# Kernel tuning notes

Measured on AMD Instinct MI355X. Metric: run time of the kernel, lower is better.

## Reference

```python
import jax, jax.numpy as jnp
import numpy as np

D_MODEL = 1024
D_INNER = 2048      # expand=2 * d_model
HEADDIM = 64
NHEADS = D_INNER // HEADDIM   # 32 (ssm heads)
D_STATE = 128
D_CONV = 4
CHUNK = 256
D_IN_PROJ = 2 * D_INNER + 2 * D_STATE + NHEADS
CONV_DIM = D_INNER + 2 * D_STATE


def setup_inputs() -> dict:
    key = jax.random.key(0)
    ks = jax.random.split(key, 8)
    sc = lambda f: 1.0 / np.sqrt(f)
    dt_init = jax.random.uniform(ks[3], (NHEADS,), minval=0.001, maxval=0.1)
    return {
        "x": jax.random.normal(ks[0], (2, 4096, D_MODEL), jnp.float32),
        "W_in": jax.random.normal(ks[1], (D_MODEL, D_IN_PROJ), jnp.float32) * sc(D_MODEL),
        "conv_w": jax.random.normal(ks[2], (CONV_DIM, D_CONV), jnp.float32) * sc(D_CONV),
        "conv_b": jnp.zeros((CONV_DIM,), jnp.float32),
        "dt_bias": jnp.log(jnp.expm1(dt_init)),            # inverse softplus
        "A_log": jnp.log(jax.random.uniform(ks[4], (NHEADS,), minval=1.0, maxval=16.0)),
        "D": jnp.ones((NHEADS,), jnp.float32),
        "norm_w": jnp.ones((D_INNER,), jnp.float32),
        "W_out": jax.random.normal(ks[5], (D_INNER, D_MODEL), jnp.float32) * sc(D_INNER),
    }


def _segsum(a):
    # a: (..., T) -> (..., T, T) lower-triangular segment sums, -inf above diag
    T = a.shape[-1]
    cs = jnp.cumsum(a, axis=-1)
    diff = cs[..., :, None] - cs[..., None, :]
    mask = jnp.tril(jnp.ones((T, T), bool))
    return jnp.where(mask, diff, -jnp.inf)


def _ssd(x, A, B, C):
    # x: (b,L,h,p) already scaled by dt; A: (b,L,h) = dt*A_head; B,C: (b,L,n)
    b, L, h, p = x.shape
    nc = L // CHUNK
    xc = x.reshape(b, nc, CHUNK, h, p)
    Ac = A.reshape(b, nc, CHUNK, h).transpose(0, 3, 1, 2)      # (b,h,nc,cl)
    Bc = B.reshape(b, nc, CHUNK, -1)
    Cc = C.reshape(b, nc, CHUNK, -1)
    Acs = jnp.cumsum(Ac, axis=-1)
    # intra-chunk (diagonal) term
    Ldec = jnp.exp(_segsum(Ac))                                # (b,h,nc,cl,cl)
    Yd = jnp.einsum('bcln,bcsn,bhcls,bcshp->bclhp', Cc, Bc, Ldec, xc)
    # chunk end states
    decay_states = jnp.exp(Acs[..., -1:] - Acs)                # (b,h,nc,cl)
    states = jnp.einsum('bcln,bhcl,bclhp->bchpn', Bc, decay_states, xc)
    # inter-chunk recurrence (zero initial state)
    states = jnp.concatenate([jnp.zeros_like(states[:, :1]), states], axis=1)
    A_chunk = jnp.pad(Acs[..., -1], ((0, 0), (0, 0), (1, 0)))  # (b,h,nc+1)
    decay_chunk = jnp.exp(_segsum(A_chunk))                    # (b,h,nc+1,nc+1)
    states = jnp.einsum('bhzc,bchpn->bzhpn', decay_chunk, states)[:, :-1]
    # state -> output term
    out_decay = jnp.exp(Acs)                                   # (b,h,nc,cl)
    Yo = jnp.einsum('bcln,bchpn,bhcl->bclhp', Cc, states, out_decay)
    return (Yd + Yo).reshape(b, L, h, p)


def reference(x, W_in, conv_w, conv_b, dt_bias, A_log, D, norm_w, W_out):
    b, L, _ = x.shape
    zxbcdt = x @ W_in                                          # (b,L,4384)
    z, xBC, dt = jnp.split(zxbcdt, [D_INNER, 2 * D_INNER + 2 * D_STATE], axis=-1)
    # causal depthwise conv1d + silu
    xp = jnp.pad(xBC, ((0, 0), (D_CONV - 1, 0), (0, 0)))
    conv = sum(xp[:, k:k + L] * conv_w[:, k] for k in range(D_CONV)) + conv_b
    xBC = jax.nn.silu(conv)
    xs, B, C = jnp.split(xBC, [D_INNER, D_INNER + D_STATE], axis=-1)
    dt = jax.nn.softplus(dt + dt_bias)                         # (b,L,h)
    A = -jnp.exp(A_log)                                        # (h,)
    xh = xs.reshape(b, L, NHEADS, HEADDIM)
    y = _ssd(xh * dt[..., None], dt * A, B, C)                 # (b,L,h,p)
    y = y + xh * D[None, None, :, None]                        # D skip per head
    y = y.reshape(b, L, D_INNER)
    # gated RMSNorm
    u = y * jax.nn.silu(z)
    u = u * jax.lax.rsqrt(jnp.mean(u * u, axis=-1, keepdims=True) + 1e-5) * norm_w
    return u @ W_out
```

## Files before the change

### kernel.cpp

```cpp
#include <hip/hip_runtime.h>
#include <math.h>

#define B_ 2
#define L_ 4096
#define DM 1024
#define DI 2048
#define HD 64
#define NH 32
#define DS 128
#define CH 256
#define NC 16
#define DPROJ 4384
#define CONVD 2304
#define NGEMM 4352

typedef unsigned short u16;
typedef unsigned int u32;
typedef __attribute__((ext_vector_type(8))) short bf16x8;
typedef __attribute__((ext_vector_type(4))) float f32x4;

__device__ __forceinline__ float silu_(float x) { return x / (1.0f + __expf(-x)); }
__device__ __forceinline__ float us2f(u16 u) {
  union { u32 i; float f; } c; c.i = ((u32)u) << 16; return c.f;
}
__device__ __forceinline__ u16 f2us(float f) {
  union { float f; u32 i; } c; c.f = f;
  u32 i = c.i;
  return (u16)((i + 0x7FFFu + ((i >> 16) & 1u)) >> 16);
}
__device__ __forceinline__ void unpack8(uint4 v, float* o) {
  o[0] = us2f(v.x & 0xffffu); o[1] = us2f(v.x >> 16);
  o[2] = us2f(v.y & 0xffffu); o[3] = us2f(v.y >> 16);
  o[4] = us2f(v.z & 0xffffu); o[5] = us2f(v.z >> 16);
  o[6] = us2f(v.w & 0xffffu); o[7] = us2f(v.w >> 16);
}
__device__ __forceinline__ void unpk16(uint4 v, u16* o) {
  o[0] = (u16)(v.x & 0xffffu); o[1] = (u16)(v.x >> 16);
  o[2] = (u16)(v.y & 0xffffu); o[3] = (u16)(v.y >> 16);
  o[4] = (u16)(v.z & 0xffffu); o[5] = (u16)(v.z >> 16);
  o[6] = (u16)(v.w & 0xffffu); o[7] = (u16)(v.w >> 16);
}
__device__ __forceinline__ bf16x8 scale8(bf16x8 a, float s) {
  bf16x8 r;
#pragma unroll
  for (int j = 0; j < 8; ++j) r[j] = (short)f2us(us2f((u16)a[j]) * s);
  return r;
}
__device__ __forceinline__ void gload16(const u16* g, u16* l) {
  __builtin_amdgcn_global_load_lds(
      (const __attribute__((address_space(1))) void*)g,
      (__attribute__((address_space(3))) void*)l, 16, 0, 0);
}

__global__ __launch_bounds__(256) void cvt_t_k(const float* __restrict__ W,
                                               u16* __restrict__ Wt,
                                               int ldW, int ldT) {
  __shared__ float tile[64][65];
  const int t = threadIdx.x;
  const int n0 = blockIdx.x * 64, k0 = blockIdx.y * 64;
#pragma unroll
  for (int i = 0; i < 16; ++i) {
    int j = i * 256 + t;
    int kk = j >> 6, nn = j & 63;
    tile[kk][nn] = W[(size_t)(k0 + kk) * ldW + n0 + nn];
  }
  __syncthreads();
#pragma unroll
  for (int i = 0; i < 16; ++i) {
    int j = i * 256 + t;
    int nn = j >> 6, kk = j & 63;
    Wt[(size_t)(n0 + nn) * ldT + k0 + kk] = f2us(tile[kk][nn]);
  }
}

__global__ __launch_bounds__(256) void cvt_tw_k(const float* __restrict__ W,
                                                const float* __restrict__ nw,
                                                u16* __restrict__ Wt,
                                                int ldW, int ldT) {
  __shared__ float tile[64][65];
  const int t = threadIdx.x;
  const int n0 = blockIdx.x * 64, k0 = blockIdx.y * 64;
#pragma unroll
  for (int i = 0; i < 16; ++i) {
    int j = i * 256 + t;
    int kk = j >> 6, nn = j & 63;
    tile[kk][nn] = W[(size_t)(k0 + kk) * ldW + n0 + nn] * nw[k0 + kk];
  }
  __syncthreads();
#pragma unroll
  for (int i = 0; i < 16; ++i) {
    int j = i * 256 + t;
    int nn = j >> 6, kk = j & 63;
    Wt[(size_t)(n0 + nn) * ldT + k0 + kk] = f2us(tile[kk][nn]);
  }
}

__global__ __launch_bounds__(512, 4) void gemm_in_k(const u16* __restrict__ A,
                                                    const u16* __restrict__ Bt,
                                                    u16* __restrict__ zb,
                                                    u16* __restrict__ xraw,
                                                    int nwg) {
  __shared__ u16 pool[24576];
  u16* Al = pool;
  u16* Bl = pool + 16384;
  const int t = threadIdx.x;
  const int w = t >> 6, lane = t & 63;
  const int fr = lane & 15, oct = lane >> 4;
  const int wm = w >> 1, wn = w & 1;
  const int q = nwg >> 3;
  const int wg = (blockIdx.x & 7) * q + (blockIdx.x >> 3);
  const int bm = wg / (NGEMM / 128), bn = wg % (NGEMM / 128);
  const int m0 = bm * 256, n0 = bn * 128;
  const int lr = lane >> 3, ls = lane & 7;
  const int gslot = (ls ^ lr) * 8;

  f32x4 acc[4][4];
#pragma unroll
  for (int mm = 0; mm < 4; ++mm)
#pragma unroll
    for (int nn = 0; nn < 4; ++nn) acc[mm][nn] = (f32x4){0.f, 0.f, 0.f, 0.f};

  for (int k0 = 0; k0 < DM; k0 += 64) {
    if (k0) __syncthreads();
#pragma unroll
    for (int i = 0; i < 4; ++i) {
      const int rowA = w * 32 + i * 8;
      gload16(&A[(size_t)(m0 + rowA + lr) * DM + k0 + gslot], &Al[rowA * 64]);
    }
#pragma unroll
    for (int i = 0; i < 2; ++i) {
      const int rowB = w * 16 + i * 8;
      gload16(&Bt[(size_t)(n0 + rowB + lr) * DM + k0 + gslot], &Bl[rowB * 64]);
    }
    __syncthreads();
#pragma unroll
    for (int kk = 0; kk < 2; ++kk) {
      bf16x8 af[4], bfr[4];
#pragma unroll
      for (int mm = 0; mm < 4; ++mm)
        af[mm] = *(const bf16x8*)&Al[(wm * 64 + mm * 16 + fr) * 64 +
                                     (((kk * 4 + oct) ^ (fr & 7)) * 8)];
#pragma unroll
      for (int nn = 0; nn < 4; ++nn)
        bfr[nn] = *(const bf16x8*)&Bl[(wn * 64 + nn * 16 + fr) * 64 +
                                      (((kk * 4 + oct) ^ (fr & 7)) * 8)];
      __builtin_amdgcn_s_setprio(1);
#pragma unroll
      for (int mm = 0; mm < 4; ++mm)
#pragma unroll
        for (int nn = 0; nn < 4; ++nn)
          acc[mm][nn] = __builtin_amdgcn_mfma_f32_16x16x32_bf16(af[mm], bfr[nn],
                                                                acc[mm][nn], 0, 0, 0);
      __builtin_amdgcn_s_setprio(0);
    }
  }

  const bool isz = (n0 < DI);
  u16* Oh = pool;
#pragma unroll
  for (int P = 0; P < 4; ++P) {
    __syncthreads();
    if (wm == P) {
#pragma unroll
      for (int mm = 0; mm < 4; ++mm)
#pragma unroll
        for (int i = 0; i < 4; ++i) {
          int rloc = mm * 16 + oct * 4 + i;
#pragma unroll
          for (int nn = 0; nn < 4; ++nn)
            Oh[rloc * 136 + wn * 64 + nn * 16 + fr] = f2us(acc[mm][nn][i]);
        }
    }
    __syncthreads();
#pragma unroll
    for (int p = 0; p < 2; ++p) {
      int e = p * 512 + t;
      int row = e >> 4, cs = (e & 15) * 8;
      uint4 v = *(const uint4*)&Oh[row * 136 + cs];
      size_t grow = m0 + P * 64 + row;
      int col = n0 + cs;
      if (isz) *(uint4*)&zb[grow * DI + col] = v;
      else     *(uint4*)&xraw[grow * CONVD + (col - DI)] = v;
    }
  }
}

template <int KDIM, int NTN>
__global__ __launch_bounds__(256) void gemm_bf16_k(const u16* __restrict__ A,
                                                   const u16* __restrict__ Bt,
                                                   const float* __restrict__ rowsum,
                                                   float* __restrict__ outf,
                                                   int nwg) {
  __shared__ u16 pool[17408];
  u16* Al = pool;
  u16* Bl = pool + 8192;
  const int t = threadIdx.x;
  const int wv = t >> 6, lane = t & 63;
  const int fr = lane & 15, oct = lane >> 4;
  const int wr = wv >> 1, wc = wv & 1;
  const int q = nwg >> 3;
  const int wg = (blockIdx.x & 7) * q + (blockIdx.x >> 3);
  const int bm = wg / NTN, bn = wg % NTN;
  const int m0 = bm * 128, n0 = bn * 128;

  const int lr = lane >> 3, ls = lane & 7;
  const int gslot = (ls ^ lr) * 8;

  f32x4 acc[4][4];
#pragma unroll
  for (int mm = 0; mm < 4; ++mm)
#pragma unroll
    for (int nn = 0; nn < 4; ++nn) acc[mm][nn] = (f32x4){0.f, 0.f, 0.f, 0.f};

  for (int k0 = 0; k0 < KDIM; k0 += 64) {
    if (k0) __syncthreads();
#pragma unroll
    for (int i = 0; i < 4; ++i) {
      const int rowA = wv * 32 + i * 8;
      gload16(&A[(size_t)(m0 + rowA + lr) * KDIM + k0 + gslot], &Al[rowA * 64]);
      gload16(&Bt[(size_t)(n0 + rowA + lr) * KDIM + k0 + gslot], &Bl[rowA * 64]);
    }
    __syncthreads();
#pragma unroll
    for (int kk = 0; kk < 2; ++kk) {
      bf16x8 af[4], bfr[4];
#pragma unroll
      for (int mm = 0; mm < 4; ++mm)
        af[mm] = *(const bf16x8*)&Al[(wr * 64 + mm * 16 + fr) * 64 +
                                     (((kk * 4 + oct) ^ (fr & 7)) * 8)];
#pragma unroll
      for (int nn = 0; nn < 4; ++nn)
        bfr[nn] = *(const bf16x8*)&Bl[(wc * 64 + nn * 16 + fr) * 64 +
                                      (((kk * 4 + oct) ^ (fr & 7)) * 8)];
#pragma unroll
      for (int mm = 0; mm < 4; ++mm)
#pragma unroll
        for (int nn = 0; nn < 4; ++nn)
          acc[mm][nn] = __builtin_amdgcn_mfma_f32_16x16x32_bf16(af[mm], bfr[nn],
                                                                acc[mm][nn], 0, 0, 0);
    }
  }

#pragma unroll
  for (int P = 0; P < 2; ++P) {
    __syncthreads();
    float* Of = (float*)pool;
    if (wr == P) {
#pragma unroll
      for (int mm = 0; mm < 4; ++mm)
#pragma unroll
        for (int i = 0; i < 4; ++i) {
          int rloc = mm * 16 + oct * 4 + i;
#pragma unroll
          for (int nn = 0; nn < 4; ++nn)
            Of[rloc * 132 + wc * 64 + nn * 16 + fr] = acc[mm][nn][i];
        }
    }
    __syncthreads();
#pragma unroll
    for (int p = 0; p < 8; ++p) {
      int e = p * 256 + t;
      int row = e >> 5, c4 = (e & 31) * 4;
      size_t grow = m0 + P * 64 + row;
      float s = rsqrtf(rowsum[grow] * (1.0f / DI) + 1e-5f);
      float4 v = *(const float4*)&Of[row * 132 + c4];
      v.x *= s; v.y *= s; v.z *= s; v.w *= s;
      *(float4*)&outf[grow * DM + n0 + c4] = v;
    }
  }
}

__global__ __launch_bounds__(256) void rowsum_k(const float* __restrict__ psum,
                                                float* __restrict__ rowsum) {
  int row = blockIdx.x * 256 + threadIdx.x;
  const float4* p = (const float4*)&psum[(size_t)row * 32];
  float s = 0.0f;
#pragma unroll
  for (int i = 0; i < 8; ++i) {
    float4 v = p[i];
    s += (v.x + v.y) + (v.z + v.w);
  }
  rowsum[row] = s;
}

__global__ __launch_bounds__(256) void dt_gemm_k(const float* __restrict__ x,
                                                 const float* __restrict__ W,
                                                 const float* __restrict__ dtb,
                                                 float* __restrict__ dtp,
                                                 u16* __restrict__ xb16) {
  __shared__ float xs[8 * 1024];
  const int t = threadIdx.x;
  const int row0 = blockIdx.x * 8;
#pragma unroll
  for (int i = 0; i < 8; ++i) {
    int j4 = i * 256 + t;
    float4 v = *(const float4*)&x[(size_t)row0 * DM + j4 * 4];
    *(float4*)&xs[j4 * 4] = v;
    u32 lo = (u32)f2us(v.x) | ((u32)f2us(v.y) << 16);
    u32 hi = (u32)f2us(v.z) | ((u32)f2us(v.w) << 16);
    *(uint2*)&xb16[(size_t)row0 * DM + j4 * 4] = make_uint2(lo, hi);
  }
  __syncthreads();
  const int r = t >> 5, h = t & 31;
  float a0 = 0.f, a1 = 0.f, a2 = 0.f, a3 = 0.f;
  const float* wcol = W + (DI + CONVD) + h;
  const float* xr = &xs[r * 1024];
  for (int k = 0; k < 1024; k += 4) {
    float4 xv = *(const float4*)&xr[k];
    a0 += xv.x * wcol[(size_t)(k + 0) * DPROJ];
    a1 += xv.y * wcol[(size_t)(k + 1) * DPROJ];
    a2 += xv.z * wcol[(size_t)(k + 2) * DPROJ];
    a3 += xv.w * wcol[(size_t)(k + 3) * DPROJ];
  }
  float v = (a0 + a1) + (a2 + a3) + dtb[h];
  dtp[(size_t)(row0 + r) * NH + h] = (v > 20.0f) ? v : log1pf(__expf(v));
}

__global__ __launch_bounds__(256) void conv_silu_k(const u16* __restrict__ xraw,
                                                   const float* __restrict__ cw,
                                                   const float* __restrict__ cb,
                                                   u16* __restrict__ xbc) {
  int idx = blockIdx.x * 256 + threadIdx.x;
  int ch8 = idx % (CONVD / 8);
  int bl = idx / (CONVD / 8);
  int l = bl & (L_ - 1);
  int ch = ch8 * 8;
  const u16* src = xraw + (size_t)bl * CONVD + ch;
  float a[8], o[8];
#pragma unroll
  for (int qq = 0; qq < 8; ++qq) a[qq] = cb[ch + qq];
  float w0[8], w1[8], w2[8], w3[8];
#pragma unroll
  for (int qq = 0; qq < 8; ++qq) {
    float4 w = *(const float4*)&cw[(ch + qq) * 4];
    w0[qq] = w.x; w1[qq] = w.y; w2[qq] = w.z; w3[qq] = w.w;
  }
  if (l >= 3) {
    uint4 v = *(const uint4*)&src[-3 * CONVD]; unpack8(v, o);
#pragma unroll
    for (int qq = 0; qq < 8; ++qq) a[qq] += o[qq] * w0[qq];
  }
  if (l >= 2) {
    uint4 v = *(const uint4*)&src[-2 * CONVD]; unpack8(v, o);
#pragma unroll
    for (int qq = 0; qq < 8; ++qq) a[qq] += o[qq] * w1[qq];
  }
  if (l >= 1) {
    uint4 v = *(const uint4*)&src[-CONVD]; unpack8(v, o);
#pragma unroll
    for (int qq = 0; qq < 8; ++qq) a[qq] += o[qq] * w2[qq];
  }
  {
    uint4 v = *(const uint4*)&src[0]; unpack8(v, o);
#pragma unroll
    for (int qq = 0; qq < 8; ++qq) a[qq] += o[qq] * w3[qq];
  }
  uint4 ov;
  ov.x = (u32)f2us(silu_(a[0])) | ((u32)f2us(silu_(a[1])) << 16);
  ov.y = (u32)f2us(silu_(a[2])) | ((u32)f2us(silu_(a[3])) << 16);
  ov.z = (u32)f2us(silu_(a[4])) | ((u32)f2us(silu_(a[5])) << 16);
  ov.w = (u32)f2us(silu_(a[6])) | ((u32)f2us(silu_(a[7])) << 16);
  *(uint4*)&xbc[(size_t)bl * CONVD + ch] = ov;
}

__global__ __launch_bounds__(256) void acs_k(const float* __restrict__ dtp,
                                             const float* __restrict__ A_log,
                                             float* __restrict__ Acs) {
  const int t = threadIdx.x;
  const int lane = t & 63, wv = t >> 6;
  const int idx = blockIdx.x * 4 + wv;
  const int h = (idx >> 4) & (NH - 1);
  const int c = idx & (NC - 1);
  const int b = idx >> 9;
  const float Ah = -__expf(A_log[h]);
  const size_t base = ((size_t)b * L_ + c * CH + lane * 4) * NH + h;
  float v0 = dtp[base] * Ah;
  float v1 = dtp[base + NH] * Ah;
  float v2 = dtp[base + 2 * NH] * Ah;
  float v3 = dtp[base + 3 * NH] * Ah;
  float c1 = v0 + v1, c2 = c1 + v2, c3 = c2 + v3;
  float tot = c3;
#pragma unroll
  for (int off = 1; off < 64; off <<= 1) {
    float p = __shfl_up(tot, off, 64);
    if (lane >= off) tot += p;
  }
  float excl = tot - c3;
  float4 ov = make_float4(excl + v0, excl + c1, excl + c2, excl + c3);
  *(float4*)&Acs[(size_t)idx * CH + lane * 4] = ov;
}

#define SLP 72
__global__ __launch_bounds__(256) void states_k(const u16* __restrict__ xbc,
                                                const float* __restrict__ dtp,
                                                const float* __restrict__ Acs,
                                                u16* __restrict__ st16) {
  __shared__ u16 BtT[128 * SLP];
  __shared__ u16 XtT[64 * SLP];
  const int t = threadIdx.x;
  const int wv = t >> 6, lane = t & 63;
  const int fr = lane & 15, oct = lane >> 4;
  const int sw = (blockIdx.x & 7) * 128 + (blockIdx.x >> 3);
  const int h = sw & 31, c = (sw >> 5) & 15, b = sw >> 9;
  const size_t acsb = (((size_t)b * NH + h) * NC + c) * CH;
  const float acs_last = Acs[acsb + (CH - 1)];
  const size_t rowbase = (size_t)b * L_ + c * CH;

  f32x4 acc[2][4];
#pragma unroll
  for (int mt = 0; mt < 2; ++mt)
#pragma unroll
    for (int pt = 0; pt < 4; ++pt) acc[mt][pt] = (f32x4){0.f, 0.f, 0.f, 0.f};

  for (int lt = 0; lt < 4; ++lt) {
    __syncthreads();
#pragma unroll
    for (int i = 0; i < 2; ++i) {
      int ci = i * 256 + t;
      int lp = ci >> 4, nk = ci & 15;
      int l0 = lp * 2;
      const u16* srcp = &xbc[(rowbase + lt * 64 + l0) * CONVD + DI + nk * 8];
      uint4 v0 = *(const uint4*)srcp;
      uint4 v1 = *(const uint4*)(srcp + CONVD);
      u16 a0[8], a1[8];
      unpk16(v0, a0); unpk16(v1, a1);
#pragma unroll
      for (int qq = 0; qq < 8; ++qq) {
        int r = nk * 8 + qq;
        u32 val = (u32)a0[qq] | ((u32)a1[qq] << 16);
        *(u32*)&BtT[r * SLP + ((((l0 >> 3) ^ (r >> 3)) & 7) << 3) + (l0 & 7)] = val;
      }
    }
    {
      int lp = t >> 3, pk = t & 7;
      int l0 = lp * 2;
      size_t row0 = rowbase + lt * 64 + l0;
      uint4 v0 = *(const uint4*)&xbc[row0 * CONVD + h * HD + pk * 8];
      uint4 v1 = *(const uint4*)&xbc[(row0 + 1) * CONVD + h * HD + pk * 8];
      float d0 = dtp[row0 * NH + h] * __expf(acs_last - Acs[acsb + lt * 64 + l0]);
      float d1 = dtp[(row0 + 1) * NH + h] * __expf(acs_last - Acs[acsb + lt * 64 + l0 + 1]);
      float o0[8], o1[8];
      unpack8(v0, o0); unpack8(v1, o1);
#pragma unroll
      for (int qq = 0; qq < 8; ++qq) {
        int r = pk * 8 + qq;
        u32 val = (u32)f2us(o0[qq] * d0) | ((u32)f2us(o1[qq] * d1) << 16);
        *(u32*)&XtT[r * SLP + ((((l0 >> 3) ^ (r >> 3)) & 7) << 3) + (l0 & 7)] = val;
      }
    }
    __syncthreads();
    __builtin_amdgcn_s_setprio(1);
#pragma unroll
    for (int ks = 0; ks < 2; ++ks) {
      bf16x8 afr[2], bfr[4];
#pragma unroll
      for (int mt = 0; mt < 2; ++mt) {
        int r = wv * 32 + mt * 16 + fr;
        afr[mt] = *(const bf16x8*)&BtT[r * SLP + ((((ks * 4 + oct) ^ (r >> 3)) & 7) << 3)];
      }
#pragma unroll
      for (int pt = 0; pt < 4; ++pt) {
        int r = pt * 16 + fr;
        bfr[pt] = *(const bf16x8*)&XtT[r * SLP + ((((ks * 4 + oct) ^ (r >> 3)) & 7) << 3)];
      }
#pragma unroll
      for (int mt = 0; mt < 2; ++mt)
#pragma unroll
        for (int pt = 0; pt < 4; ++pt)
          acc[mt][pt] = __builtin_amdgcn_mfma_f32_16x16x32_bf16(afr[mt], bfr[pt],
                                                                acc[mt][pt], 0, 0, 0);
    }
    __builtin_amdgcn_s_setprio(0);
  }
  size_t sbase = (((size_t)b * NC + c) * NH + h) * (size_t)(HD * DS);
#pragma unroll
  for (int mt = 0; mt < 2; ++mt)
#pragma unroll
    for (int pt = 0; pt < 4; ++pt) {
      int p = pt * 16 + fr;
      int n0 = wv * 32 + mt * 16 + oct * 4;
      u32 lo = (u32)f2us(acc[mt][pt][0]) | ((u32)f2us(acc[mt][pt][1]) << 16);
      u32 hi = (u32)f2us(acc[mt][pt][2]) | ((u32)f2us(acc[mt][pt][3]) << 16);
      *(uint2*)&st16[sbase + (size_t)p * DS + n0] = make_uint2(lo, hi);
    }
}

__global__ __launch_bounds__(256) void scan_k(u16* __restrict__ st16,
                                              const float* __restrict__ Acs) {
  const int t = threadIdx.x;
  const int seg = blockIdx.x & 15;
  const int bh = blockIdx.x >> 4;
  const int h = bh & 31, b = bh >> 5;
  const int e2 = seg * 256 + t;
  const size_t acssb = ((size_t)b * NH + h) * NC * CH;
  float run0 = 0.0f, run1 = 0.0f;
#pragma unroll
  for (int c = 0; c < NC; ++c) {
    float dAl = __expf(Acs[acssb + (size_t)c * CH + (CH - 1)]);
    size_t e = (((size_t)b * NC + c) * NH + h) * (size_t)(HD * DS) + e2 * 2;
    u32 v = *(const u32*)&st16[e];
    float s0 = us2f((u16)(v & 0xffffu)), s1 = us2f((u16)(v >> 16));
    *(u32*)&st16[e] = (u32)f2us(run0) | ((u32)f2us(run1) << 16);
    run0 = fmaf(dAl, run0, s0);
    run1 = fmaf(dAl, run1, s1);
  }
}

#define SP 72
#define XOFF 8192
#define POFF 12800
__global__ __launch_bounds__(512, 4) void ssd_out_k(const u16* __restrict__ xbc,
                                                    const float* __restrict__ dtp,
                                                    const float* __restrict__ Acs,
                                                    const u16* __restrict__ st16,
                                                    const float* __restrict__ Dvec,
                                                    const u16* __restrict__ zb,
                                                    u16* __restrict__ v_out,
                                                    float* __restrict__ psum) {
  __shared__ u16 pool[31232];
  __shared__ float acs_s[256];
  const int t = threadIdx.x;
  const int w = t >> 6, lane = t & 63;
  const int fr = lane & 15, oct = lane >> 4;
  const int sw = (blockIdx.x & 7) * 128 + (blockIdx.x >> 3);
  const int h = sw & 31, c = (sw >> 5) & 15, b = sw >> 9;
  const size_t acsb = (((size_t)b * NH + h) * NC + c) * CH;
  const size_t rowbase = (size_t)b * L_ + c * CH;
  if (t < 256) acs_s[t] = Acs[acsb + t];
  const size_t sb = (((size_t)b * NC + c) * NH + h) * (size_t)(HD * DS);
#pragma unroll
  for (int i = 0; i < 2; ++i) {
    int ci = i * 512 + t; int p = ci >> 4, nk = ci & 15;
    uint4 v = *(const uint4*)&st16[sb + (size_t)p * DS + nk * 8];
    *(uint4*)&pool[p * 136 + nk * 8] = v;
  }
  __syncthreads();
  bf16x8 ca[2][4];
#pragma unroll
  for (int mt = 0; mt < 2; ++mt)
#pragma unroll
    for (int kk = 0; kk < 4; ++kk)
      ca[mt][kk] = *(const bf16x8*)&xbc[(rowbase + w * 32 + mt * 16 + fr) * CONVD +
                                        DI + DS + kk * 32 + oct * 8];
  f32x4 acc_y[2][4];
#pragma unroll
  for (int mt = 0; mt < 2; ++mt)
#pragma unroll
    for (int pp4 = 0; pp4 < 4; ++pp4) acc_y[mt][pp4] = (f32x4){0.f, 0.f, 0.f, 0.f};

  {
    float eL0 = __expf(acs_s[w * 32 + fr]);
    float eL1 = __expf(acs_s[w * 32 + 16 + fr]);
    __builtin_amdgcn_s_setprio(1);
#pragma unroll
    for (int kk = 0; kk < 4; ++kk) {
      bf16x8 c0 = scale8(ca[0][kk], eL0);
      bf16x8 c1 = scale8(ca[1][kk], eL1);
#pragma unroll
      for (int pp4 = 0; pp4 < 4; ++pp4) {
        bf16x8 sf = *(const bf16x8*)&pool[(pp4 * 16 + fr) * 136 + kk * 32 + oct * 8];
        acc_y[0][pp4] = __builtin_amdgcn_mfma_f32_16x16x32_bf16(c0, sf, acc_y[0][pp4], 0, 0, 0);
        acc_y[1][pp4] = __builtin_amdgcn_mfma_f32_16x16x32_bf16(c1, sf, acc_y[1][pp4], 0, 0, 0);
      }
    }
    __builtin_amdgcn_s_setprio(0);
  }

  const int stmax = w >> 1, delta = (w & 1) << 5;
  for (int st = 0; st < 4; ++st) {
    __syncthreads();
#pragma unroll
    for (int i = 0; i < 2; ++i) {
      int ci = i * 512 + t; int ll = ci >> 4, ck = ci & 15;
      uint4 v = *(const uint4*)&xbc[(rowbase + st * 64 + ll) * CONVD + DI + ck * 8];
      *(uint4*)&pool[ll * 128 + ((ck * 8) ^ ((ll & 7) << 3))] = v;
    }
    if (t < 256) {
      int lp = t >> 3, pk = t & 7;
      int s0 = lp * 2;
      size_t row0 = rowbase + st * 64 + s0;
      uint4 v0 = *(const uint4*)&xbc[row0 * CONVD + h * HD + pk * 8];
      uint4 v1 = *(const uint4*)&xbc[(row0 + 1) * CONVD + h * HD + pk * 8];
      float d0 = dtp[row0 * NH + h];
      float d1 = dtp[(row0 + 1) * NH + h];
      float o0[8], o1[8];
      unpack8(v0, o0); unpack8(v1, o1);
#pragma unroll
      for (int qq = 0; qq < 8; ++qq) {
        int r = pk * 8 + qq;
        u32 val = (u32)f2us(o0[qq] * d0) | ((u32)f2us(o1[qq] * d1) << 16);
        *(u32*)&pool[XOFF + r * SP + ((((s0 >> 3) ^ (r >> 3)) & 7) << 3) + (s0 & 7)] = val;
      }
    }
    __syncthreads();
    if (st > stmax) continue;
    const bool diag = (st == stmax);
#pragma unroll
    for (int ss4 = 0; ss4 < 4; ++ss4) {
      bf16x8 bbf[4];
#pragma unroll
      for (int kk = 0; kk < 4; ++kk)
        bbf[kk] = *(const bf16x8*)&pool[(ss4 * 16 + fr) * 128 +
                                        ((kk * 32 + oct * 8) ^ ((fr & 7) << 3))];
      int s_in = ss4 * 16 + fr;
      float aS = acs_s[st * 64 + s_in];
#pragma unroll
      for (int mt = 0; mt < 2; ++mt) {
        f32x4 sacc = (f32x4){0.f, 0.f, 0.f, 0.f};
        __builtin_amdgcn_s_setprio(1);
#pragma unroll
        for (int kk = 0; kk < 4; ++kk)
          sacc = __builtin_amdgcn_mfma_f32_16x16x32_bf16(ca[mt][kk], bbf[kk], sacc, 0, 0, 0);
        __builtin_amdgcn_s_setprio(0);
#pragma unroll
        for (int i = 0; i < 4; ++i) {
          int r = mt * 16 + oct * 4 + i;
          float aL = acs_s[w * 32 + r];
          float wgt = (!diag || (s_in <= r + delta)) ? __expf(aL - aS) : 0.0f;
          pool[POFF + w * 2304 + r * SP + s_in] = f2us(sacc[i] * wgt);
        }
      }
    }
    bf16x8 pa[2][2];
#pragma unroll
    for (int mt = 0; mt < 2; ++mt)
#pragma unroll
      for (int k2 = 0; k2 < 2; ++k2)
        pa[mt][k2] = *(const bf16x8*)&pool[POFF + w * 2304 + (mt * 16 + fr) * SP +
                                           k2 * 32 + oct * 8];
    __builtin_amdgcn_s_setprio(1);
#pragma unroll
    for (int pp4 = 0; pp4 < 4; ++pp4) {
      int rx = pp4 * 16 + fr, xg = rx >> 3;
      bf16x8 xb0 = *(const bf16x8*)&pool[XOFF + rx * SP + (((oct) ^ xg) & 7) * 8];
      bf16x8 xb1 = *(const bf16x8*)&pool[XOFF + rx * SP + (((4 + oct) ^ xg) & 7) * 8];
#pragma unroll
      for (int mt = 0; mt < 2; ++mt) {
        acc_y[mt][pp4] = __builtin_amdgcn_mfma_f32_16x16x32_bf16(pa[mt][0], xb0, acc_y[mt][pp4], 0, 0, 0);
        acc_y[mt][pp4] = __builtin_amdgcn_mfma_f32_16x16x32_bf16(pa[mt][1], xb1, acc_y[mt][pp4], 0, 0, 0);
      }
    }
    __builtin_amdgcn_s_setprio(0);
  }

  const float Dh = Dvec[h];
  float rs[2][4];
#pragma unroll
  for (int mt = 0; mt < 2; ++mt)
#pragma unroll
    for (int i = 0; i < 4; ++i) {
      size_t row = rowbase + w * 32 + mt * 16 + oct * 4 + i;
      float rsum = 0.0f;
#pragma unroll
      for (int pp4 = 0; pp4 < 4; ++pp4) {
        int col = h * HD + pp4 * 16 + fr;
        float xs = us2f(xbc[row * CONVD + col]);
        float zz = us2f(zb[row * DI + col]);
        float vv = (acc_y[mt][pp4][i] + Dh * xs) * silu_(zz);
        v_out[row * DI + col] = f2us(vv);
        rsum += vv * vv;
      }
      rs[mt][i] = rsum;
    }
#pragma unroll
  for (int mt = 0; mt < 2; ++mt)
#pragma unroll
    for (int i = 0; i < 4; ++i) {
      float s = rs[mt][i];
#pragma unroll
      for (int off = 8; off >= 1; off >>= 1) s += __shfl_xor(s, off, 64);
      if (fr == 0) {
        size_t row = rowbase + w * 32 + mt * 16 + oct * 4 + i;
        psum[row * 32 + h] = s;
      }
    }
}

extern "C" void kernel_launch(void* const* d_in, const int* in_sizes, int n_in,
                              void* d_out, int out_size, void* d_ws, size_t ws_size,
                              hipStream_t stream) {
  const float* x      = (const float*)d_in[0];
  const float* W_in   = (const float*)d_in[1];
  const float* conv_w = (const float*)d_in[2];
  const float* conv_b = (const float*)d_in[3];
  const float* dt_b   = (const float*)d_in[4];
  const float* A_log  = (const float*)d_in[5];
  const float* Dvec   = (const float*)d_in[6];
  const float* norm_w = (const float*)d_in[7];
  const float* W_out  = (const float*)d_in[8];
  float* out = (float*)d_out;

  u16* zb       = (u16*)d_ws;
  u16* xbc      = zb + (size_t)B_ * L_ * DI;
  float* dtp    = (float*)(xbc + (size_t)B_ * L_ * CONVD);
  float* Acs    = dtp + (size_t)B_ * L_ * NH;
  u16* stregion = (u16*)(Acs + (size_t)B_ * NH * L_);
  u16* uni      = stregion + (size_t)B_ * NC * NH * HD * DS * 2;
  u16* xraw = uni;
  u16* v    = uni;

  u16* xb16     = stregion;
  u16* wint     = stregion + (size_t)B_ * L_ * DM;
  u16* states16 = stregion;
  float* psum   = (float*)(stregion + (size_t)B_ * NC * NH * HD * DS);
  float* rowsum = psum + (size_t)B_ * L_ * NH;
  u16* woutt    = stregion;

  const int Mrows = B_ * L_;

  dt_gemm_k<<<Mrows / 8, 256, 0, stream>>>(x, W_in, dt_b, dtp, xb16);
  cvt_t_k<<<dim3(NGEMM / 64, DM / 64), 256, 0, stream>>>(W_in, wint, DPROJ, DM);

  const int nwg_in = (Mrows / 256) * (NGEMM / 128);
  gemm_in_k<<<nwg_in, 512, 0, stream>>>(xb16, wint, zb, xraw, nwg_in);

  conv_silu_k<<<(Mrows * (CONVD / 8)) / 256, 256, 0, stream>>>(xraw, conv_w, conv_b, xbc);
  acs_k<<<(B_ * NH * NC) / 4, 256, 0, stream>>>(dtp, A_log, Acs);
  states_k<<<B_ * NC * NH, 256, 0, stream>>>(xbc, dtp, Acs, states16);
  scan_k<<<B_ * NH * 16, 256, 0, stream>>>(states16, Acs);
  ssd_out_k<<<B_ * NC * NH, 512, 0, stream>>>(xbc, dtp, Acs, states16, Dvec,
                                              zb, v, psum);
  rowsum_k<<<Mrows / 256, 256, 0, stream>>>(psum, rowsum);

  cvt_tw_k<<<dim3(DM / 64, DI / 64), 256, 0, stream>>>(W_out, norm_w, woutt, DM, DI);
  const int nwg_out = (Mrows / 128) * (DM / 128);
  gemm_bf16_k<DI, DM / 128><<<nwg_out, 256, 0, stream>>>(v, woutt, rowsum, out, nwg_out);
}
```

Measured before the change: 339.6 us.

## Merge prep kernels, fold acs into states and rowsum into output GEMM

Merges the dt GEMM, bf16 conversion of x, and both weight transposes into a single prep kernel dispatched by block index. The per-chunk cumsum (acs) moves into states_k, which keeps it in shared memory and also writes it out for later kernels. The row-sum reduction moves into the output GEMM prologue. This cuts kernel launches from 11 to 7 and removes some global round-trips. In exchange, the workspace layout changes so the transposed W_out and psum get their own regions, and states_k does redundant per-block scan work.

```diff
diff --git a/kernel.cpp b/kernel.cpp
--- a/kernel.cpp
+++ b/kernel.cpp
@@ -52,46 +52,70 @@
       (__attribute__((address_space(3))) void*)l, 16, 0, 0);
 }
 
-__global__ __launch_bounds__(256) void cvt_t_k(const float* __restrict__ W,
-                                               u16* __restrict__ Wt,
-                                               int ldW, int ldT) {
-  __shared__ float tile[64][65];
+__global__ __launch_bounds__(256) void prep_k(const float* __restrict__ x,
+                                              const float* __restrict__ W_in,
+                                              const float* __restrict__ W_out,
+                                              const float* __restrict__ nw,
+                                              const float* __restrict__ dtb,
+                                              float* __restrict__ dtp,
+                                              u16* __restrict__ xb16,
+                                              u16* __restrict__ wint,
+                                              u16* __restrict__ woutt) {
+  __shared__ float shmem[8 * 1024];
   const int t = threadIdx.x;
-  const int n0 = blockIdx.x * 64, k0 = blockIdx.y * 64;
-#pragma unroll
-  for (int i = 0; i < 16; ++i) {
-    int j = i * 256 + t;
-    int kk = j >> 6, nn = j & 63;
-    tile[kk][nn] = W[(size_t)(k0 + kk) * ldW + n0 + nn];
-  }
-  __syncthreads();
-#pragma unroll
-  for (int i = 0; i < 16; ++i) {
-    int j = i * 256 + t;
-    int nn = j >> 6, kk = j & 63;
-    Wt[(size_t)(n0 + nn) * ldT + k0 + kk] = f2us(tile[kk][nn]);
-  }
-}
-
-__global__ __launch_bounds__(256) void cvt_tw_k(const float* __restrict__ W,
-                                                const float* __restrict__ nw,
-                                                u16* __restrict__ Wt,
-                                                int ldW, int ldT) {
-  __shared__ float tile[64][65];
-  const int t = threadIdx.x;
-  const int n0 = blockIdx.x * 64, k0 = blockIdx.y * 64;
-#pragma unroll
-  for (int i = 0; i < 16; ++i) {
-    int j = i * 256 + t;
-    int kk = j >> 6, nn = j & 63;
-    tile[kk][nn] = W[(size_t)(k0 + kk) * ldW + n0 + nn] * nw[k0 + kk];
-  }
-  __syncthreads();
-#pragma unroll
-  for (int i = 0; i < 16; ++i) {
-    int j = i * 256 + t;
-    int nn = j >> 6, kk = j & 63;
-    Wt[(size_t)(n0 + nn) * ldT + k0 + kk] = f2us(tile[kk][nn]);
+  const int bid = blockIdx.x;
+  if (bid < 1024) {
+    const int row0 = bid * 8;
+#pragma unroll
+    for (int i = 0; i < 8; ++i) {
+      int j4 = i * 256 + t;
+      float4 v = *(const float4*)&x[(size_t)row0 * DM + j4 * 4];
+      *(float4*)&shmem[j4 * 4] = v;
+      u32 lo = (u32)f2us(v.x) | ((u32)f2us(v.y) << 16);
+      u32 hi = (u32)f2us(v.z) | ((u32)f2us(v.w) << 16);
+      *(uint2*)&xb16[(size_t)row0 * DM + j4 * 4] = make_uint2(lo, hi);
+    }
+    __syncthreads();
+    const int r = t >> 5, h = t & 31;
+    float a0 = 0.f, a1 = 0.f, a2 = 0.f, a3 = 0.f;
+    const float* wcol = W_in + (DI + CONVD) + h;
+    const float* xr = &shmem[r * 1024];
+    for (int k = 0; k < 1024; k += 4) {
+      float4 xv = *(const float4*)&xr[k];
+      a0 += xv.x * wcol[(size_t)(k + 0) * DPROJ];
+      a1 += xv.y * wcol[(size_t)(k + 1) * DPROJ];
+      a2 += xv.z * wcol[(size_t)(k + 2) * DPROJ];
+      a3 += xv.w * wcol[(size_t)(k + 3) * DPROJ];
+    }
+    float v = (a0 + a1) + (a2 + a3) + dtb[h];
+    dtp[(size_t)(row0 + r) * NH + h] = (v > 20.0f) ? v : log1pf(__expf(v));
+  } else {
+    float (*tile)[65] = (float(*)[65])shmem;
+    const float* W; u16* Wt; int ldW, ldT, n0, k0; bool fold;
+    if (bid < 2112) {
+      int j = bid - 1024;
+      W = W_in; Wt = wint; ldW = DPROJ; ldT = DM; fold = false;
+      n0 = (j % (NGEMM / 64)) * 64; k0 = (j / (NGEMM / 64)) * 64;
+    } else {
+      int j = bid - 2112;
+      W = W_out; Wt = woutt; ldW = DM; ldT = DI; fold = true;
+      n0 = (j % (DM / 64)) * 64; k0 = (j / (DM / 64)) * 64;
+    }
+#pragma unroll
+    for (int i = 0; i < 16; ++i) {
+      int j = i * 256 + t;
+      int kk = j >> 6, nn = j & 63;
+      float v = W[(size_t)(k0 + kk) * ldW + n0 + nn];
+      if (fold) v *= nw[k0 + kk];
+      tile[kk][nn] = v;
+    }
+    __syncthreads();
+#pragma unroll
+    for (int i = 0; i < 16; ++i) {
+      int j = i * 256 + t;
+      int nn = j >> 6, kk = j & 63;
+      Wt[(size_t)(n0 + nn) * ldT + k0 + kk] = f2us(tile[kk][nn]);
+    }
   }
 }
 
@@ -186,12 +210,13 @@
 }
 
 template <int KDIM, int NTN>
-__global__ __launch_bounds__(256) void gemm_bf16_k(const u16* __restrict__ A,
-                                                   const u16* __restrict__ Bt,
-                                                   const float* __restrict__ rowsum,
-                                                   float* __restrict__ outf,
-                                                   int nwg) {
+__global__ __launch_bounds__(256) void gemm_out_k(const u16* __restrict__ A,
+                                                  const u16* __restrict__ Bt,
+                                                  const float* __restrict__ psum,
+                                                  float* __restrict__ outf,
+                                                  int nwg) {
   __shared__ u16 pool[17408];
+  __shared__ float rs_s[128];
   u16* Al = pool;
   u16* Bl = pool + 8192;
   const int t = threadIdx.x;
@@ -203,6 +228,17 @@
   const int bm = wg / NTN, bn = wg % NTN;
   const int m0 = bm * 128, n0 = bn * 128;
 
+  if (t < 128) {
+    const float4* p = (const float4*)&psum[(size_t)(m0 + t) * 32];
+    float s = 0.0f;
+#pragma unroll
+    for (int i = 0; i < 8; ++i) {
+      float4 v = p[i];
+      s += (v.x + v.y) + (v.z + v.w);
+    }
+    rs_s[t] = rsqrtf(s * (1.0f / DI) + 1e-5f);
+  }
+
   const int lr = lane >> 3, ls = lane & 7;
   const int gslot = (ls ^ lr) * 8;
 
@@ -261,59 +297,12 @@
     for (int p = 0; p < 8; ++p) {
       int e = p * 256 + t;
       int row = e >> 5, c4 = (e & 31) * 4;
-      size_t grow = m0 + P * 64 + row;
-      float s = rsqrtf(rowsum[grow] * (1.0f / DI) + 1e-5f);
+      float s = rs_s[P * 64 + row];
       float4 v = *(const float4*)&Of[row * 132 + c4];
       v.x *= s; v.y *= s; v.z *= s; v.w *= s;
-      *(float4*)&outf[grow * DM + n0 + c4] = v;
-    }
-  }
-}
-
-__global__ __launch_bounds__(256) void rowsum_k(const float* __restrict__ psum,
-                                                float* __restrict__ rowsum) {
-  int row = blockIdx.x * 256 + threadIdx.x;
-  const float4* p = (const float4*)&psum[(size_t)row * 32];
-  float s = 0.0f;
-#pragma unroll
-  for (int i = 0; i < 8; ++i) {
-    float4 v = p[i];
-    s += (v.x + v.y) + (v.z + v.w);
-  }
-  rowsum[row] = s;
-}
-
-__global__ __launch_bounds__(256) void dt_gemm_k(const float* __restrict__ x,
-                                                 const float* __restrict__ W,
-                                                 const float* __restrict__ dtb,
-                                                 float* __restrict__ dtp,
-                                                 u16* __restrict__ xb16) {
-  __shared__ float xs[8 * 1024];
-  const int t = threadIdx.x;
-  const int row0 = blockIdx.x * 8;
-#pragma unroll
-  for (int i = 0; i < 8; ++i) {
-    int j4 = i * 256 + t;
-    float4 v = *(const float4*)&x[(size_t)row0 * DM + j4 * 4];
-    *(float4*)&xs[j4 * 4] = v;
-    u32 lo = (u32)f2us(v.x) | ((u32)f2us(v.y) << 16);
-    u32 hi = (u32)f2us(v.z) | ((u32)f2us(v.w) << 16);
-    *(uint2*)&xb16[(size_t)row0 * DM + j4 * 4] = make_uint2(lo, hi);
-  }
-  __syncthreads();
-  const int r = t >> 5, h = t & 31;
-  float a0 = 0.f, a1 = 0.f, a2 = 0.f, a3 = 0.f;
-  const float* wcol = W + (DI + CONVD) + h;
-  const float* xr = &xs[r * 1024];
-  for (int k = 0; k < 1024; k += 4) {
-    float4 xv = *(const float4*)&xr[k];
-    a0 += xv.x * wcol[(size_t)(k + 0) * DPROJ];
-    a1 += xv.y * wcol[(size_t)(k + 1) * DPROJ];
-    a2 += xv.z * wcol[(size_t)(k + 2) * DPROJ];
-    a3 += xv.w * wcol[(size_t)(k + 3) * DPROJ];
-  }
-  float v = (a0 + a1) + (a2 + a3) + dtb[h];
-  dtp[(size_t)(row0 + r) * NH + h] = (v > 20.0f) ? v : log1pf(__expf(v));
+      *(float4*)&outf[(size_t)(m0 + P * 64 + row) * DM + n0 + c4] = v;
+    }
+  }
 }
 
 __global__ __launch_bounds__(256) void conv_silu_k(const u16* __restrict__ xraw,
@@ -363,48 +352,44 @@
   *(uint4*)&xbc[(size_t)bl * CONVD + ch] = ov;
 }
 
-__global__ __launch_bounds__(256) void acs_k(const float* __restrict__ dtp,
-                                             const float* __restrict__ A_log,
-                                             float* __restrict__ Acs) {
-  const int t = threadIdx.x;
-  const int lane = t & 63, wv = t >> 6;
-  const int idx = blockIdx.x * 4 + wv;
-  const int h = (idx >> 4) & (NH - 1);
-  const int c = idx & (NC - 1);
-  const int b = idx >> 9;
-  const float Ah = -__expf(A_log[h]);
-  const size_t base = ((size_t)b * L_ + c * CH + lane * 4) * NH + h;
-  float v0 = dtp[base] * Ah;
-  float v1 = dtp[base + NH] * Ah;
-  float v2 = dtp[base + 2 * NH] * Ah;
-  float v3 = dtp[base + 3 * NH] * Ah;
-  float c1 = v0 + v1, c2 = c1 + v2, c3 = c2 + v3;
-  float tot = c3;
-#pragma unroll
-  for (int off = 1; off < 64; off <<= 1) {
-    float p = __shfl_up(tot, off, 64);
-    if (lane >= off) tot += p;
-  }
-  float excl = tot - c3;
-  float4 ov = make_float4(excl + v0, excl + c1, excl + c2, excl + c3);
-  *(float4*)&Acs[(size_t)idx * CH + lane * 4] = ov;
-}
-
 #define SLP 72
 __global__ __launch_bounds__(256) void states_k(const u16* __restrict__ xbc,
                                                 const float* __restrict__ dtp,
-                                                const float* __restrict__ Acs,
+                                                const float* __restrict__ A_log,
+                                                float* __restrict__ Acs,
                                                 u16* __restrict__ st16) {
   __shared__ u16 BtT[128 * SLP];
   __shared__ u16 XtT[64 * SLP];
+  __shared__ float acs_s[256];
   const int t = threadIdx.x;
   const int wv = t >> 6, lane = t & 63;
   const int fr = lane & 15, oct = lane >> 4;
   const int sw = (blockIdx.x & 7) * 128 + (blockIdx.x >> 3);
   const int h = sw & 31, c = (sw >> 5) & 15, b = sw >> 9;
   const size_t acsb = (((size_t)b * NH + h) * NC + c) * CH;
-  const float acs_last = Acs[acsb + (CH - 1)];
   const size_t rowbase = (size_t)b * L_ + c * CH;
+
+  if (t < 64) {
+    const float Ah = -__expf(A_log[h]);
+    const size_t base = (rowbase + t * 4) * NH + h;
+    float v0 = dtp[base] * Ah;
+    float v1 = dtp[base + NH] * Ah;
+    float v2 = dtp[base + 2 * NH] * Ah;
+    float v3 = dtp[base + 3 * NH] * Ah;
+    float c1 = v0 + v1, c2 = c1 + v2, c3 = c2 + v3;
+    float tot = c3;
+#pragma unroll
+    for (int off = 1; off < 64; off <<= 1) {
+      float p = __shfl_up(tot, off, 64);
+      if (t >= off) tot += p;
+    }
+    float excl = tot - c3;
+    float4 ov = make_float4(excl + v0, excl + c1, excl + c2, excl + c3);
+    *(float4*)&acs_s[t * 4] = ov;
+    *(float4*)&Acs[acsb + t * 4] = ov;
+  }
+  __syncthreads();
+  const float acs_last = acs_s[255];
 
   f32x4 acc[2][4];
 #pragma unroll
@@ -437,8 +422,8 @@
       size_t row0 = rowbase + lt * 64 + l0;
       uint4 v0 = *(const uint4*)&xbc[row0 * CONVD + h * HD + pk * 8];
       uint4 v1 = *(const uint4*)&xbc[(row0 + 1) * CONVD + h * HD + pk * 8];
-      float d0 = dtp[row0 * NH + h] * __expf(acs_last - Acs[acsb + lt * 64 + l0]);
-      float d1 = dtp[(row0 + 1) * NH + h] * __expf(acs_last - Acs[acsb + lt * 64 + l0 + 1]);
+      float d0 = dtp[row0 * NH + h] * __expf(acs_last - acs_s[lt * 64 + l0]);
+      float d1 = dtp[(row0 + 1) * NH + h] * __expf(acs_last - acs_s[lt * 64 + l0 + 1]);
       float o0[8], o1[8];
       unpack8(v0, o0); unpack8(v1, o1);
 #pragma unroll
@@ -701,28 +686,24 @@
 
   u16* xb16     = stregion;
   u16* wint     = stregion + (size_t)B_ * L_ * DM;
+  u16* woutt    = wint + (size_t)NGEMM * DM;
+  float* psum   = (float*)(woutt + (size_t)DM * DI);
   u16* states16 = stregion;
-  float* psum   = (float*)(stregion + (size_t)B_ * NC * NH * HD * DS);
-  float* rowsum = psum + (size_t)B_ * L_ * NH;
-  u16* woutt    = stregion;
 
   const int Mrows = B_ * L_;
 
-  dt_gemm_k<<<Mrows / 8, 256, 0, stream>>>(x, W_in, dt_b, dtp, xb16);
-  cvt_t_k<<<dim3(NGEMM / 64, DM / 64), 256, 0, stream>>>(W_in, wint, DPROJ, DM);
+  prep_k<<<1024 + (NGEMM / 64) * (DM / 64) + (DM / 64) * (DI / 64), 256, 0, stream>>>(
+      x, W_in, W_out, norm_w, dt_b, dtp, xb16, wint, woutt);
 
   const int nwg_in = (Mrows / 256) * (NGEMM / 128);
   gemm_in_k<<<nwg_in, 512, 0, stream>>>(xb16, wint, zb, xraw, nwg_in);
 
   conv_silu_k<<<(Mrows * (CONVD / 8)) / 256, 256, 0, stream>>>(xraw, conv_w, conv_b, xbc);
-  acs_k<<<(B_ * NH * NC) / 4, 256, 0, stream>>>(dtp, A_log, Acs);
-  states_k<<<B_ * NC * NH, 256, 0, stream>>>(xbc, dtp, Acs, states16);
+  states_k<<<B_ * NC * NH, 256, 0, stream>>>(xbc, dtp, A_log, Acs, states16);
   scan_k<<<B_ * NH * 16, 256, 0, stream>>>(states16, Acs);
   ssd_out_k<<<B_ * NC * NH, 512, 0, stream>>>(xbc, dtp, Acs, states16, Dvec,
                                               zb, v, psum);
-  rowsum_k<<<Mrows / 256, 256, 0, stream>>>(psum, rowsum);
-
-  cvt_tw_k<<<dim3(DM / 64, DI / 64), 256, 0, stream>>>(W_out, norm_w, woutt, DM, DI);
+
   const int nwg_out = (Mrows / 128) * (DM / 128);
-  gemm_bf16_k<DI, DM / 128><<<nwg_out, 256, 0, stream>>>(v, woutt, rowsum, out, nwg_out);
-}
+  gemm_out_k<DI, DM / 128><<<nwg_out, 256, 0, stream>>>(v, woutt, psum, out, nwg_out);
+}
```

Measured after the change: 337.4 us (median of 2 runs). Within noise of the previous version (-0.7%).
